# Kernel tuning notes

Measured on AMD Instinct MI355X. Metric: run time of the kernel, lower is better.

The kernel has to match this reference:

```python
import jax, jax.numpy as jnp
import numpy as np

N, E, G, ND, H, C, L = 100000, 640000, 1000, 128, 128, 10, 4
ATOMS_PER_GRAPH = 100  # N = G * ATOMS_PER_GRAPH
NEG_SLOPE = 0.01  # nn.LeakyReLU default


def setup_inputs() -> dict:
    key = jax.random.key(0)
    ks = jax.random.split(key, 16)
    s = 0.05
    return {
        "node_attr": jax.random.normal(ks[0], (N, ND), jnp.float32),
        "edge_index": jax.random.randint(ks[1], (2, E), 0, N, jnp.int64),
        "num_atoms": jnp.full((G,), ATOMS_PER_GRAPH, dtype=jnp.int64),
        "enc_W": jax.random.normal(ks[2], (ND, H), jnp.float32) * s,
        "enc_b": jnp.zeros((H,), jnp.float32),
        "gcn_W": jax.random.normal(ks[3], (L, H, H), jnp.float32) * s,
        "gcn_b": jnp.zeros((L, H), jnp.float32),
        "r_W1": jax.random.normal(ks[4], (H, H), jnp.float32) * s,
        "r_b1": jnp.zeros((H,), jnp.float32),
        "r_W2": jax.random.normal(ks[5], (H, H), jnp.float32) * s,
        "r_b2": jnp.zeros((H,), jnp.float32),
        "s_W1": jax.random.normal(ks[6], (H, H), jnp.float32) * s,
        "s_b1": jnp.zeros((H,), jnp.float32),
        "s_W2": jax.random.normal(ks[7], (H, H), jnp.float32) * s,
        "s_b2": jnp.zeros((H,), jnp.float32),
        "fin_W": jax.random.normal(ks[8], (H, C), jnp.float32) * s,
        "fin_b": jnp.zeros((C,), jnp.float32),
    }


def _leaky(x):
    return jnp.where(x > 0, x, NEG_SLOPE * x)


def reference(node_attr, edge_index, num_atoms, enc_W, enc_b, gcn_W, gcn_b,
              r_W1, r_b1, r_W2, r_b2, s_W1, s_b1, s_W2, s_b2, fin_W, fin_b):
    dst, src = edge_index[0], edge_index[1]
    # degree normalization constant across layers: deg(i) = in-edge count, divide by deg+1
    deg = jax.ops.segment_sum(jnp.ones((E,), node_attr.dtype), dst, num_segments=N)
    inv_deg = 1.0 / (deg + 1.0)  # [N]

    x = node_attr @ enc_W + enc_b  # [N, H]
    for l in range(L):
        h = x @ gcn_W[l] + gcn_b[l]
        agg = jax.ops.segment_sum(h[src], dst, num_segments=N)  # scatter_sum over dst
        x = (h + agg) * inv_deg[:, None]

    # GateMLP: ReLuMLP(x) * SigmoidMLP(x)
    r = _leaky(_leaky(x @ r_W1 + r_b1) @ r_W2 + r_b2)
    g = jax.nn.sigmoid(_leaky(x @ s_W1 + s_b1) @ s_W2 + s_b2)
    x = r * g  # [N, H]

    # graph pooling: scatter_mean over graph ids
    graph_mask = jnp.repeat(jnp.arange(G), num_atoms, total_repeat_length=N)
    gsum = jax.ops.segment_sum(x, graph_mask, num_segments=G)
    cnt = jax.ops.segment_sum(jnp.ones((N,), x.dtype), graph_mask, num_segments=G)
    graph_attr = gsum / jnp.maximum(cnt, 1.0)[:, None]  # [G, H]
    return graph_attr @ fin_W + fin_b  # [G, C]
```

## Files before the change

### kernel.cpp

```cpp
#include <hip/hip_runtime.h>
#include <hip/hip_bf16.h>
#include <cstddef>
#include <cstdint>

#define CAP 40
#define LEAK 0.01f

typedef __attribute__((ext_vector_type(8))) short short8v;
typedef __attribute__((ext_vector_type(4))) float float4v;

__device__ __forceinline__ unsigned short f2bf(float f) {
    uint32_t u = __float_as_uint(f);
    uint32_t r = (u + 0x7FFFu + ((u >> 16) & 1u)) >> 16;
    return (unsigned short)r;
}
__device__ __forceinline__ float bf2f(unsigned short s) {
    return __uint_as_float(((uint32_t)s) << 16);
}

__global__ void build_buckets(const int* __restrict__ ei, int E_,
                              int* __restrict__ cnt, int* __restrict__ bucket) {
    int e = (blockIdx.x * 256 + threadIdx.x) * 4;
    if (e >= E_) return;
    if (e + 4 <= E_) {
        int4 d4 = *(const int4*)&ei[e];
        int4 s4 = *(const int4*)&ei[(size_t)E_ + e];
        int p0 = atomicAdd(&cnt[d4.x], 1);
        int p1 = atomicAdd(&cnt[d4.y], 1);
        int p2 = atomicAdd(&cnt[d4.z], 1);
        int p3 = atomicAdd(&cnt[d4.w], 1);
        if (p0 < CAP) bucket[(size_t)d4.x * CAP + p0] = s4.x;
        if (p1 < CAP) bucket[(size_t)d4.y * CAP + p1] = s4.y;
        if (p2 < CAP) bucket[(size_t)d4.z * CAP + p2] = s4.z;
        if (p3 < CAP) bucket[(size_t)d4.w * CAP + p3] = s4.w;
    } else {
        for (; e < E_; ++e) {
            int d = ei[e], s = ei[(size_t)E_ + e];
            int p = atomicAdd(&cnt[d], 1);
            if (p < CAP) bucket[(size_t)d * CAP + p] = s;
        }
    }
}

__global__ void pack_w(const float* __restrict__ enc, const float* __restrict__ gcn,
                       const float* __restrict__ rw1, const float* __restrict__ rw2,
                       const float* __restrict__ sw1, const float* __restrict__ sw2,
                       unsigned short* __restrict__ p) {
    int m = blockIdx.x >> 3;
    int idx = (blockIdx.x & 7) * 256 + threadIdx.x;
    const float* W;
    switch (m) {
        case 0: W = enc; break;
        case 1: case 2: case 3: case 4: W = gcn + (size_t)(m - 1) * 16384; break;
        case 5: W = rw1; break;
        case 6: W = rw2; break;
        case 7: W = sw1; break;
        default: W = sw2; break;
    }
    int n = idx & 127;
    int fg = (idx >> 7) & 3;
    int kc = idx >> 9;
    short8v v;
#pragma unroll
    for (int j = 0; j < 8; ++j)
        v[j] = (short)f2bf(W[(size_t)(kc * 32 + fg * 8 + j) * 128 + n]);
    *(short8v*)(p + (size_t)m * 16384 + (size_t)idx * 8) = v;
}

__device__ __forceinline__ void load_wf(const unsigned short* __restrict__ Wpack,
                                        int w, int fr, int fg, short8v wf[2][4]) {
    const short8v* Wp = (const short8v*)Wpack;
#pragma unroll
    for (int t = 0; t < 2; ++t)
#pragma unroll
        for (int kc = 0; kc < 4; ++kc)
            wf[t][kc] = Wp[(kc * 4 + fg) * 128 + w * 32 + t * 16 + fr];
}

__device__ __forceinline__ void mfma_tile(const unsigned short* As, int fr, int fg,
                                          const short8v wf[2][4], float4v acc[4][2]) {
#pragma unroll
    for (int m = 0; m < 4; ++m) {
        acc[m][0] = (float4v){0.f, 0.f, 0.f, 0.f};
        acc[m][1] = (float4v){0.f, 0.f, 0.f, 0.f};
    }
#pragma unroll
    for (int kc = 0; kc < 4; ++kc) {
        short8v a[4];
#pragma unroll
        for (int m = 0; m < 4; ++m) {
            int row = m * 16 + fr;
            int cb = (kc * 64 + fg * 16) ^ ((row & 7) << 4);
            a[m] = *(const short8v*)((const char*)As + row * 256 + cb);
        }
#pragma unroll
        for (int m = 0; m < 4; ++m) {
            acc[m][0] = __builtin_amdgcn_mfma_f32_16x16x32_bf16(a[m], wf[0][kc], acc[m][0], 0, 0, 0);
            acc[m][1] = __builtin_amdgcn_mfma_f32_16x16x32_bf16(a[m], wf[1][kc], acc[m][1], 0, 0, 0);
        }
    }
}

__global__ __launch_bounds__(256) void gemm_enc(const float* __restrict__ Ain,
                                                const unsigned short* __restrict__ Wpack,
                                                const float* __restrict__ bias,
                                                unsigned short* __restrict__ Cout, int M) {
    __shared__ unsigned short As[64 * 128];
    const int tid = threadIdx.x;
    const int lane = tid & 63;
    const int w = tid >> 6;
    const int row0 = blockIdx.x * 64;
    const int fr = lane & 15;
    const int fg = lane >> 4;

    short8v wf[2][4];
    load_wf(Wpack, w, fr, fg, wf);

    {
        const int r = tid >> 2;
        const int cg = tid & 3;
        const int row = row0 + r;
        char* lbase = (char*)As + r * 256;
        const float* Ap = Ain + (size_t)row * 128 + cg * 32;
#pragma unroll
        for (int i = 0; i < 4; ++i) {
            short8v v = {0, 0, 0, 0, 0, 0, 0, 0};
            if (row < M) {
                float4v p = *(const float4v*)(Ap + i * 8);
                float4v q = *(const float4v*)(Ap + i * 8 + 4);
                v[0] = (short)f2bf(p[0]); v[1] = (short)f2bf(p[1]);
                v[2] = (short)f2bf(p[2]); v[3] = (short)f2bf(p[3]);
                v[4] = (short)f2bf(q[0]); v[5] = (short)f2bf(q[1]);
                v[6] = (short)f2bf(q[2]); v[7] = (short)f2bf(q[3]);
            }
            int cb = (cg * 64 + i * 16) ^ ((r & 7) << 4);
            *(short8v*)(lbase + cb) = v;
        }
    }
    __syncthreads();

    float4v acc[4][2];
    mfma_tile(As, fr, fg, wf, acc);

#pragma unroll
    for (int t = 0; t < 2; ++t) {
        const int col = w * 32 + t * 16 + fr;
        const float bv = bias[col];
#pragma unroll
        for (int m = 0; m < 4; ++m)
#pragma unroll
            for (int q = 0; q < 4; ++q) {
                int row = row0 + m * 16 + fg * 4 + q;
                if (row < M) Cout[(size_t)row * 128 + col] = f2bf(acc[m][t][q] + bv);
            }
    }
}

__device__ __forceinline__ void acc8(float a[8], uint4 v, float m) {
    a[0] = fmaf(m, bf2f((unsigned short)(v.x & 0xffff)), a[0]);
    a[1] = fmaf(m, bf2f((unsigned short)(v.x >> 16)), a[1]);
    a[2] = fmaf(m, bf2f((unsigned short)(v.y & 0xffff)), a[2]);
    a[3] = fmaf(m, bf2f((unsigned short)(v.y >> 16)), a[3]);
    a[4] = fmaf(m, bf2f((unsigned short)(v.z & 0xffff)), a[4]);
    a[5] = fmaf(m, bf2f((unsigned short)(v.z >> 16)), a[5]);
    a[6] = fmaf(m, bf2f((unsigned short)(v.w & 0xffff)), a[6]);
    a[7] = fmaf(m, bf2f((unsigned short)(v.w >> 16)), a[7]);
}

__global__ __launch_bounds__(256) void gcn_fused(const unsigned short* __restrict__ x,
                                                 const int* __restrict__ bucket,
                                                 const int* __restrict__ cnt,
                                                 const unsigned short* __restrict__ Wpack,
                                                 const float* __restrict__ bias,
                                                 unsigned short* __restrict__ xout,
                                                 int Nn) {
    __shared__ unsigned short As[64 * 128];
    const int tid = threadIdx.x;
    const int lane = tid & 63;
    const int w = tid >> 6;
    const int row0 = blockIdx.x * 64;
    const int fr = lane & 15;
    const int fg = lane >> 4;
    const int l16 = lane & 15;
    const int g = lane >> 4;
    const int gl = lane & 48;
    const char* xb = (const char*)x;

    int cfull = 0;
    if (lane < 16) {
        int gn = row0 + w * 16 + lane;
        if (gn >= Nn) gn = Nn - 1;
        cfull = cnt[gn];
    }
    uint4 own[4];
    int2 pre[4];
#pragma unroll
    for (int p = 0; p < 4; ++p) {
        int gn = row0 + w * 16 + p * 4 + g;
        if (gn >= Nn) gn = Nn - 1;
        own[p] = *(const uint4*)(xb + (size_t)gn * 256 + l16 * 16);
        pre[p] = *(const int2*)&bucket[(size_t)gn * CAP + 2 * l16];
    }

#pragma unroll
    for (int p = 0; p < 4; ++p) {
        const int n = p * 4 + g;
        const int r = w * 16 + n;
        const int dfull = __shfl(cfull, n);
        const float id = 1.0f / (float)(dfull + 1);
        const int d = min(dfull, CAP);
        const int dm = min(d, 32);

        float a[8];
        acc8(a, own[p], 0.f);
        {
            uint4 o = own[p];
            a[0] = bf2f((unsigned short)(o.x & 0xffff));
            a[1] = bf2f((unsigned short)(o.x >> 16));
            a[2] = bf2f((unsigned short)(o.y & 0xffff));
            a[3] = bf2f((unsigned short)(o.y >> 16));
            a[4] = bf2f((unsigned short)(o.z & 0xffff));
            a[5] = bf2f((unsigned short)(o.z >> 16));
            a[6] = bf2f((unsigned short)(o.w & 0xffff));
            a[7] = bf2f((unsigned short)(o.w >> 16));
        }

        for (int j = 0; j < dm; j += 4) {
            int sl = gl + (j >> 1);
            int s0 = __shfl(pre[p].x, sl);
            int s1 = __shfl(pre[p].y, sl);
            int s2 = __shfl(pre[p].x, sl + 1);
            int s3 = __shfl(pre[p].y, sl + 1);
            s0 = min(max(s0, 0), Nn - 1);
            s1 = min(max(s1, 0), Nn - 1);
            s2 = min(max(s2, 0), Nn - 1);
            s3 = min(max(s3, 0), Nn - 1);
            uint4 v0 = *(const uint4*)(xb + (size_t)s0 * 256 + l16 * 16);
            uint4 v1 = *(const uint4*)(xb + (size_t)s1 * 256 + l16 * 16);
            uint4 v2 = *(const uint4*)(xb + (size_t)s2 * 256 + l16 * 16);
            uint4 v3 = *(const uint4*)(xb + (size_t)s3 * 256 + l16 * 16);
            acc8(a, v0, (j + 0 < d) ? 1.f : 0.f);
            acc8(a, v1, (j + 1 < d) ? 1.f : 0.f);
            acc8(a, v2, (j + 2 < d) ? 1.f : 0.f);
            acc8(a, v3, (j + 3 < d) ? 1.f : 0.f);
        }
        if (d > 32) {
            int gn = row0 + r; if (gn >= Nn) gn = Nn - 1;
            for (int j = 32; j < d; ++j) {
                int s = bucket[(size_t)gn * CAP + j];
                uint4 v = *(const uint4*)(xb + (size_t)s * 256 + l16 * 16);
                acc8(a, v, 1.f);
            }
        }

#pragma unroll
        for (int i = 0; i < 8; ++i) a[i] *= id;
        uint4 o;
        o.x = (uint32_t)f2bf(a[0]) | ((uint32_t)f2bf(a[1]) << 16);
        o.y = (uint32_t)f2bf(a[2]) | ((uint32_t)f2bf(a[3]) << 16);
        o.z = (uint32_t)f2bf(a[4]) | ((uint32_t)f2bf(a[5]) << 16);
        o.w = (uint32_t)f2bf(a[6]) | ((uint32_t)f2bf(a[7]) << 16);
        *(uint4*)((char*)As + r * 256 + ((l16 * 16) ^ ((r & 7) << 4))) = o;
    }

    short8v wf[2][4];
    load_wf(Wpack, w, fr, fg, wf);
    __syncthreads();

    float4v acc[4][2];
    mfma_tile(As, fr, fg, wf, acc);

#pragma unroll
    for (int t = 0; t < 2; ++t) {
        const int col = w * 32 + t * 16 + fr;
        const float bv = bias[col];
#pragma unroll
        for (int m = 0; m < 4; ++m)
#pragma unroll
            for (int q = 0; q < 4; ++q) {
                int row = row0 + m * 16 + fg * 4 + q;
                if (row < Nn) xout[(size_t)row * 128 + col] = f2bf(acc[m][t][q] + bv);
            }
    }
}

__global__ __launch_bounds__(256) void gate_fused(const unsigned short* __restrict__ x,
                                                  const unsigned short* __restrict__ wpack,
                                                  const float* __restrict__ rb1,
                                                  const float* __restrict__ rb2,
                                                  const float* __restrict__ sb1,
                                                  const float* __restrict__ sb2,
                                                  unsigned short* __restrict__ out, int M) {
    __shared__ unsigned short As[64 * 128];
    __shared__ unsigned short Bs[64 * 128];
    const int tid = threadIdx.x;
    const int lane = tid & 63;
    const int w = tid >> 6;
    const int row0 = blockIdx.x * 64;
    const int fr = lane & 15;
    const int fg = lane >> 4;

    {
        const int r = tid >> 2;
        const int cg = tid & 3;
        const int row = row0 + r;
        char* lbase = (char*)As + r * 256;
        const unsigned short* Ap = x + (size_t)row * 128 + cg * 32;
#pragma unroll
        for (int i = 0; i < 4; ++i) {
            short8v v = {0, 0, 0, 0, 0, 0, 0, 0};
            if (row < M) v = *(const short8v*)(Ap + i * 8);
            int cb = (cg * 64 + i * 16) ^ ((r & 7) << 4);
            *(short8v*)(lbase + cb) = v;
        }
    }
    __syncthreads();

    short8v wf[2][4];
    float4v acc[4][2];

#define WRITE_LDS_LEAKY(BIAS)                                                          \
    {                                                                                  \
        _Pragma("unroll") for (int t = 0; t < 2; ++t) {                                \
            const int col = w * 32 + t * 16 + fr;                                      \
            const float bv = (BIAS)[col];                                              \
            _Pragma("unroll") for (int m = 0; m < 4; ++m)                              \
                _Pragma("unroll") for (int q = 0; q < 4; ++q) {                        \
                    int r_ = m * 16 + fg * 4 + q;                                      \
                    float v_ = acc[m][t][q] + bv;                                      \
                    v_ = v_ > 0.f ? v_ : LEAK * v_;                                    \
                    *(unsigned short*)((char*)Bs + r_ * 256 +                          \
                                       ((col * 2) ^ ((r_ & 7) << 4))) = f2bf(v_);      \
                }                                                                      \
        }                                                                              \
    }

    load_wf(wpack + (size_t)5 * 16384, w, fr, fg, wf);
    mfma_tile(As, fr, fg, wf, acc);
    WRITE_LDS_LEAKY(rb1);
    __syncthreads();

    load_wf(wpack + (size_t)6 * 16384, w, fr, fg, wf);
    float4v racc[4][2];
    mfma_tile(Bs, fr, fg, wf, racc);
#pragma unroll
    for (int t = 0; t < 2; ++t) {
        const float bv = rb2[w * 32 + t * 16 + fr];
#pragma unroll
        for (int m = 0; m < 4; ++m)
#pragma unroll
            for (int q = 0; q < 4; ++q) {
                float v = racc[m][t][q] + bv;
                racc[m][t][q] = v > 0.f ? v : LEAK * v;
            }
    }
    __syncthreads();

    load_wf(wpack + (size_t)7 * 16384, w, fr, fg, wf);
    mfma_tile(As, fr, fg, wf, acc);
    WRITE_LDS_LEAKY(sb1);
    __syncthreads();

    load_wf(wpack + (size_t)8 * 16384, w, fr, fg, wf);
    mfma_tile(Bs, fr, fg, wf, acc);
#pragma unroll
    for (int t = 0; t < 2; ++t) {
        const int col = w * 32 + t * 16 + fr;
        const float bv = sb2[col];
#pragma unroll
        for (int m = 0; m < 4; ++m)
#pragma unroll
            for (int q = 0; q < 4; ++q) {
                int row = row0 + m * 16 + fg * 4 + q;
                if (row < M) {
                    float gg = 1.f / (1.f + __expf(-(acc[m][t][q] + bv)));
                    out[(size_t)row * 128 + col] = f2bf(gg * racc[m][t][q]);
                }
            }
    }
#undef WRITE_LDS_LEAKY
}

__global__ void scan_atoms(const int* __restrict__ na, int* __restrict__ goff, int G_) {
    __shared__ int sh[1024];
    int t = threadIdx.x;
    int v = (t < G_) ? na[t] : 0;
    sh[t] = v;
    __syncthreads();
    for (int ofs = 1; ofs < 1024; ofs <<= 1) {
        int u = (t >= ofs) ? sh[t - ofs] : 0;
        __syncthreads();
        sh[t] += u;
        __syncthreads();
    }
    if (t == 0) goff[0] = 0;
    if (t < G_) goff[t + 1] = sh[t];
}

__global__ void pool(const unsigned short* __restrict__ x, const int* __restrict__ goff,
                     float* __restrict__ gattr, int G_) {
    int g = blockIdx.x * 2 + (threadIdx.x >> 7);
    if (g >= G_) return;
    int d = threadIdx.x & 127;
    int a0 = goff[g], a1 = goff[g + 1];
    float s0 = 0.f, s1 = 0.f, s2 = 0.f, s3 = 0.f;
    int a = a0;
    for (; a + 4 <= a1; a += 4) {
        s0 += bf2f(x[(size_t)(a + 0) * 128 + d]);
        s1 += bf2f(x[(size_t)(a + 1) * 128 + d]);
        s2 += bf2f(x[(size_t)(a + 2) * 128 + d]);
        s3 += bf2f(x[(size_t)(a + 3) * 128 + d]);
    }
    for (; a < a1; ++a) s0 += bf2f(x[(size_t)a * 128 + d]);
    float s = (s0 + s1) + (s2 + s3);
    float c = (float)max(a1 - a0, 1);
    gattr[(size_t)g * 128 + d] = s / c;
}

__global__ void final_gemm(const float* __restrict__ gattr, const float* __restrict__ fW,
                           const float* __restrict__ fb, float* __restrict__ out,
                           int G_, int C_) {
    int i = blockIdx.x * 256 + threadIdx.x;
    if (i >= G_ * C_) return;
    int g = i / C_, c = i % C_;
    const float* row = gattr + (size_t)g * 128;
    float s = fb[c];
    for (int k = 0; k < 128; ++k) s = fmaf(row[k], fW[k * C_ + c], s);
    out[i] = s;
}

extern "C" void kernel_launch(void* const* d_in, const int* in_sizes, int n_in,
                              void* d_out, int out_size, void* d_ws, size_t ws_size,
                              hipStream_t stream) {
    const float* node_attr = (const float*)d_in[0];
    const int* edge_index  = (const int*)d_in[1];
    const int* num_atoms   = (const int*)d_in[2];
    const float* enc_W = (const float*)d_in[3];
    const float* enc_b = (const float*)d_in[4];
    const float* gcn_W = (const float*)d_in[5];
    const float* gcn_b = (const float*)d_in[6];
    const float* r_W1 = (const float*)d_in[7];
    const float* r_b1 = (const float*)d_in[8];
    const float* r_W2 = (const float*)d_in[9];
    const float* r_b2 = (const float*)d_in[10];
    const float* s_W1 = (const float*)d_in[11];
    const float* s_b1 = (const float*)d_in[12];
    const float* s_W2 = (const float*)d_in[13];
    const float* s_b2 = (const float*)d_in[14];
    const float* fin_W = (const float*)d_in[15];
    const float* fin_b = (const float*)d_in[16];
    float* out = (float*)d_out;

    const int N_ = in_sizes[0] / 128;
    const int E_ = in_sizes[1] / 2;
    const int G_ = in_sizes[2];
    const int C_ = in_sizes[16];

    size_t off = 0;
    auto alloc = [&](size_t bytes) -> void* {
        void* p = (char*)d_ws + off;
        off += (bytes + 255) & ~(size_t)255;
        return p;
    };
    unsigned short* bx = (unsigned short*)alloc((size_t)N_ * 128 * 2);
    unsigned short* bh = (unsigned short*)alloc((size_t)N_ * 128 * 2);
    int* bucket = (int*)alloc((size_t)N_ * CAP * 4);
    int* cnt    = (int*)alloc((size_t)N_ * 4);
    unsigned short* wpack = (unsigned short*)alloc((size_t)9 * 16384 * 2);
    int* goff   = (int*)alloc((size_t)(G_ + 1) * 4);
    float* gattr = (float*)alloc((size_t)G_ * 128 * 4);
    (void)ws_size; (void)n_in; (void)out_size;

    const int gemm_grid = (N_ + 63) / 64;

    hipMemsetAsync(cnt, 0, (size_t)N_ * 4, stream);
    build_buckets<<<(E_ / 4 + 255) / 256, 256, 0, stream>>>(edge_index, E_, cnt, bucket);
    pack_w<<<72, 256, 0, stream>>>(enc_W, gcn_W, r_W1, r_W2, s_W1, s_W2, wpack);
    scan_atoms<<<1, 1024, 0, stream>>>(num_atoms, goff, G_);

    gemm_enc<<<gemm_grid, 256, 0, stream>>>(node_attr, wpack, enc_b, bx, N_);

    unsigned short* cur = bx;
    unsigned short* nxt = bh;
    for (int l = 0; l < 4; ++l) {
        gcn_fused<<<gemm_grid, 256, 0, stream>>>(cur, bucket, cnt,
                                                 wpack + (size_t)(1 + l) * 16384,
                                                 gcn_b + (size_t)l * 128, nxt, N_);
        unsigned short* t = cur; cur = nxt; nxt = t;
    }

    gate_fused<<<gemm_grid, 256, 0, stream>>>(cur, wpack, r_b1, r_b2, s_b1, s_b2, nxt, N_);

    pool<<<(G_ + 1) / 2, 256, 0, stream>>>(nxt, goff, gattr, G_);
    final_gemm<<<(G_ * C_ + 255) / 256, 256, 0, stream>>>(gattr, fin_W, fin_b, out, G_, C_);
}
```

Baseline: 297.8 us.

## Restructure gate MLP to keep activations in registers and stage weights in LDS

The gate kernel now has each wave own 16 rows, holding input fragments in registers. Full 128x128 weight matrices are staged into shared memory one at a time, and the first-layer outputs are passed to the second GEMM through cross-lane shuffles instead of an LDS round-trip. This removes the per-block A/B activation tiles and the intermediate LDS writes, at the cost of more weight staging and barriers. The GCN kernel also gets a min-blocks launch bound of 4 and drops a redundant accumulator initialisation.

```diff
diff --git a/kernel.cpp b/kernel.cpp
--- a/kernel.cpp
+++ b/kernel.cpp
@@ -16,6 +16,12 @@
 }
 __device__ __forceinline__ float bf2f(unsigned short s) {
     return __uint_as_float(((uint32_t)s) << 16);
+}
+__device__ __forceinline__ short8v frag_from_pairs(uint32_t p0, uint32_t p1,
+                                                   uint32_t p2, uint32_t p3) {
+    union { uint32_t u[4]; short8v v; } c;
+    c.u[0] = p0; c.u[1] = p1; c.u[2] = p2; c.u[3] = p3;
+    return c.v;
 }
 
 __global__ void build_buckets(const int* __restrict__ ei, int E_,
@@ -167,13 +173,13 @@
     a[7] = fmaf(m, bf2f((unsigned short)(v.w >> 16)), a[7]);
 }
 
-__global__ __launch_bounds__(256) void gcn_fused(const unsigned short* __restrict__ x,
-                                                 const int* __restrict__ bucket,
-                                                 const int* __restrict__ cnt,
-                                                 const unsigned short* __restrict__ Wpack,
-                                                 const float* __restrict__ bias,
-                                                 unsigned short* __restrict__ xout,
-                                                 int Nn) {
+__global__ __launch_bounds__(256, 4) void gcn_fused(const unsigned short* __restrict__ x,
+                                                    const int* __restrict__ bucket,
+                                                    const int* __restrict__ cnt,
+                                                    const unsigned short* __restrict__ Wpack,
+                                                    const float* __restrict__ bias,
+                                                    unsigned short* __restrict__ xout,
+                                                    int Nn) {
     __shared__ unsigned short As[64 * 128];
     const int tid = threadIdx.x;
     const int lane = tid & 63;
@@ -212,7 +218,6 @@
         const int dm = min(d, 32);
 
         float a[8];
-        acc8(a, own[p], 0.f);
         {
             uint4 o = own[p];
             a[0] = bf2f((unsigned short)(o.x & 0xffff));
@@ -291,94 +296,120 @@
                                                   const float* __restrict__ sb1,
                                                   const float* __restrict__ sb2,
                                                   unsigned short* __restrict__ out, int M) {
-    __shared__ unsigned short As[64 * 128];
-    __shared__ unsigned short Bs[64 * 128];
+    __shared__ unsigned short Ws[128 * 128];
     const int tid = threadIdx.x;
     const int lane = tid & 63;
     const int w = tid >> 6;
-    const int row0 = blockIdx.x * 64;
-    const int fr = lane & 15;
+    const int l16 = lane & 15;
     const int fg = lane >> 4;
-
-    {
-        const int r = tid >> 2;
-        const int cg = tid & 3;
-        const int row = row0 + r;
-        char* lbase = (char*)As + r * 256;
-        const unsigned short* Ap = x + (size_t)row * 128 + cg * 32;
-#pragma unroll
-        for (int i = 0; i < 4; ++i) {
-            short8v v = {0, 0, 0, 0, 0, 0, 0, 0};
-            if (row < M) v = *(const short8v*)(Ap + i * 8);
-            int cb = (cg * 64 + i * 16) ^ ((r & 7) << 4);
-            *(short8v*)(lbase + cb) = v;
-        }
-    }
+    const int row0 = blockIdx.x * 64 + w * 16;
+
+    int xr = row0 + l16;
+    if (xr >= M) xr = M - 1;
+    short8v xbf[4];
+#pragma unroll
+    for (int kc = 0; kc < 4; ++kc)
+        xbf[kc] = *(const short8v*)(x + (size_t)xr * 128 + kc * 32 + fg * 8);
+
+    const short8v* WL = (const short8v*)Ws;
+    uint32_t upR[8][2], upS[8][2];
+
+#define STAGE(mi)                                                             \
+    {                                                                         \
+        const short8v* src = (const short8v*)(wpack + (size_t)(mi) * 16384);  \
+        short8v* dst = (short8v*)Ws;                                          \
+        _Pragma("unroll") for (int i = 0; i < 8; ++i)                         \
+            dst[i * 256 + tid] = src[i * 256 + tid];                          \
+    }
+
+#define PASS1(BIAS, UP)                                                       \
+    _Pragma("unroll") for (int nt = 0; nt < 8; ++nt) {                        \
+        float4v acc = (float4v){0.f, 0.f, 0.f, 0.f};                          \
+        _Pragma("unroll") for (int kc = 0; kc < 4; ++kc)                      \
+            acc = __builtin_amdgcn_mfma_f32_16x16x32_bf16(                    \
+                WL[(kc * 4 + fg) * 128 + nt * 16 + l16], xbf[kc], acc, 0, 0, 0); \
+        _Pragma("unroll") for (int q = 0; q < 4; ++q) {                       \
+            float v = acc[q] + (BIAS)[nt * 16 + fg * 4 + q];                  \
+            acc[q] = v > 0.f ? v : LEAK * v;                                  \
+        }                                                                     \
+        UP[nt][0] = (uint32_t)f2bf(acc[0]) | ((uint32_t)f2bf(acc[1]) << 16);  \
+        UP[nt][1] = (uint32_t)f2bf(acc[2]) | ((uint32_t)f2bf(acc[3]) << 16);  \
+    }
+
+#define MKUF(UP, UF)                                                          \
+    _Pragma("unroll") for (int kc = 0; kc < 4; ++kc) {                        \
+        uint32_t pr0, pr1, pr2, pr3;                                          \
+        {                                                                     \
+            int srcl = (((2 * fg + 0) & 3) << 4) + l16;                       \
+            uint32_t lo = __shfl((int)UP[2 * kc][0], srcl);                   \
+            uint32_t hi = __shfl((int)UP[2 * kc + 1][0], srcl);               \
+            pr0 = (fg & 2) ? hi : lo;                                         \
+            lo = __shfl((int)UP[2 * kc][1], srcl);                            \
+            hi = __shfl((int)UP[2 * kc + 1][1], srcl);                        \
+            pr1 = (fg & 2) ? hi : lo;                                         \
+        }                                                                     \
+        {                                                                     \
+            int srcl = (((2 * fg + 1) & 3) << 4) + l16;                       \
+            uint32_t lo = __shfl((int)UP[2 * kc][0], srcl);                   \
+            uint32_t hi = __shfl((int)UP[2 * kc + 1][0], srcl);               \
+            pr2 = (fg & 2) ? hi : lo;                                         \
+            lo = __shfl((int)UP[2 * kc][1], srcl);                            \
+            hi = __shfl((int)UP[2 * kc + 1][1], srcl);                        \
+            pr3 = (fg & 2) ? hi : lo;                                         \
+        }                                                                     \
+        UF[kc] = frag_from_pairs(pr0, pr1, pr2, pr3);                         \
+    }
+
+#define PASS2(UF, ACCOUT)                                                     \
+    _Pragma("unroll") for (int t2 = 0; t2 < 8; ++t2) {                        \
+        float4v acc = (float4v){0.f, 0.f, 0.f, 0.f};                          \
+        _Pragma("unroll") for (int kc = 0; kc < 4; ++kc)                      \
+            acc = __builtin_amdgcn_mfma_f32_16x16x32_bf16(                    \
+                UF[kc], WL[(kc * 4 + fg) * 128 + t2 * 16 + l16], acc, 0, 0, 0); \
+        ACCOUT[t2] = acc;                                                     \
+    }
+
+    STAGE(5); __syncthreads();
+    PASS1(rb1, upR);
     __syncthreads();
-
-    short8v wf[2][4];
-    float4v acc[4][2];
-
-#define WRITE_LDS_LEAKY(BIAS)                                                          \
-    {                                                                                  \
-        _Pragma("unroll") for (int t = 0; t < 2; ++t) {                                \
-            const int col = w * 32 + t * 16 + fr;                                      \
-            const float bv = (BIAS)[col];                                              \
-            _Pragma("unroll") for (int m = 0; m < 4; ++m)                              \
-                _Pragma("unroll") for (int q = 0; q < 4; ++q) {                        \
-                    int r_ = m * 16 + fg * 4 + q;                                      \
-                    float v_ = acc[m][t][q] + bv;                                      \
-                    v_ = v_ > 0.f ? v_ : LEAK * v_;                                    \
-                    *(unsigned short*)((char*)Bs + r_ * 256 +                          \
-                                       ((col * 2) ^ ((r_ & 7) << 4))) = f2bf(v_);      \
-                }                                                                      \
-        }                                                                              \
-    }
-
-    load_wf(wpack + (size_t)5 * 16384, w, fr, fg, wf);
-    mfma_tile(As, fr, fg, wf, acc);
-    WRITE_LDS_LEAKY(rb1);
+    STAGE(7); __syncthreads();
+    PASS1(sb1, upS);
     __syncthreads();
-
-    load_wf(wpack + (size_t)6 * 16384, w, fr, fg, wf);
-    float4v racc[4][2];
-    mfma_tile(Bs, fr, fg, wf, racc);
-#pragma unroll
-    for (int t = 0; t < 2; ++t) {
-        const float bv = rb2[w * 32 + t * 16 + fr];
-#pragma unroll
-        for (int m = 0; m < 4; ++m)
-#pragma unroll
-            for (int q = 0; q < 4; ++q) {
-                float v = racc[m][t][q] + bv;
-                racc[m][t][q] = v > 0.f ? v : LEAK * v;
+    STAGE(6); __syncthreads();
+    short8v uf[4];
+    MKUF(upR, uf);
+    float4v rf[8];
+    PASS2(uf, rf);
+#pragma unroll
+    for (int t2 = 0; t2 < 8; ++t2) {
+        float bv = rb2[t2 * 16 + l16];
+#pragma unroll
+        for (int q = 0; q < 4; ++q) {
+            float v = rf[t2][q] + bv;
+            rf[t2][q] = v > 0.f ? v : LEAK * v;
+        }
+    }
+    __syncthreads();
+    STAGE(8); __syncthreads();
+    MKUF(upS, uf);
+    float4v gacc[8];
+    PASS2(uf, gacc);
+#pragma unroll
+    for (int t2 = 0; t2 < 8; ++t2) {
+        float bv = sb2[t2 * 16 + l16];
+#pragma unroll
+        for (int q = 0; q < 4; ++q) {
+            int row = row0 + fg * 4 + q;
+            if (row < M) {
+                float gg = 1.f / (1.f + __expf(-(gacc[t2][q] + bv)));
+                out[(size_t)row * 128 + t2 * 16 + l16] = f2bf(gg * rf[t2][q]);
             }
-    }
-    __syncthreads();
-
-    load_wf(wpack + (size_t)7 * 16384, w, fr, fg, wf);
-    mfma_tile(As, fr, fg, wf, acc);
-    WRITE_LDS_LEAKY(sb1);
-    __syncthreads();
-
-    load_wf(wpack + (size_t)8 * 16384, w, fr, fg, wf);
-    mfma_tile(Bs, fr, fg, wf, acc);
-#pragma unroll
-    for (int t = 0; t < 2; ++t) {
-        const int col = w * 32 + t * 16 + fr;
-        const float bv = sb2[col];
-#pragma unroll
-        for (int m = 0; m < 4; ++m)
-#pragma unroll
-            for (int q = 0; q < 4; ++q) {
-                int row = row0 + m * 16 + fg * 4 + q;
-                if (row < M) {
-                    float gg = 1.f / (1.f + __expf(-(acc[m][t][q] + bv)));
-                    out[(size_t)row * 128 + col] = f2bf(gg * racc[m][t][q]);
-                }
-            }
-    }
-#undef WRITE_LDS_LEAKY
+        }
+    }
+#undef STAGE
+#undef PASS1
+#undef MKUF
+#undef PASS2
 }
 
 __global__ void scan_atoms(const int* __restrict__ na, int* __restrict__ goff, int G_) {
```

Result: slower. 305.1 us (+2.4%).
